# Optimization experiments

Hardware: AMD Instinct MI355X
Metric: run time of the kernel (lower is better)

## Reference

```python
import jax, jax.numpy as jnp
import numpy as np

B = 512       # batch
D = 256       # n_embd
NH = 4        # heads
NN = 8 * D // NH   # neurons per head = 512
NTOT = NH * NN     # 2048
DH = D // NH       # 64
K = 8              # thinking steps
EPS_LN = 1e-5


def _ln(x, g, b):
    mu = jnp.mean(x, axis=-1, keepdims=True)
    var = jnp.mean((x - mu) ** 2, axis=-1, keepdims=True)
    return (x - mu) * jax.lax.rsqrt(var + EPS_LN) * g + b


def setup_inputs() -> dict:
    key = jax.random.key(0)
    ks = jax.random.split(key, 12)
    s = 0.02
    w = lambda k, shape: (jax.random.normal(k, shape, jnp.float32) * s)
    return {
        "boards": jax.random.normal(ks[0], (B, 12, 8, 8), jnp.float32),
        # board_encoder: Linear(768,d) -> GELU -> LN(d) -> Linear(d,d); weights stored (in,out)
        "enc_w1": w(ks[1], (768, D)), "enc_b1": jnp.zeros((D,), jnp.float32),
        "enc_ln_g": jnp.ones((D,), jnp.float32), "enc_ln_b": jnp.zeros((D,), jnp.float32),
        "enc_w2": w(ks[2], (D, D)), "enc_b2": jnp.zeros((D,), jnp.float32),
        "xinit_w": w(ks[3], (D, NTOT)), "xinit_b": jnp.zeros((NTOT,), jnp.float32),
        "D_y": w(ks[4], (NH, D, NN)),
        "E": w(ks[5], (NTOT, D)),
        "D_x": w(ks[6], (NH, D, NN)),
        "By_w": w(ks[7], (D, D)),
        "Bx_w": w(ks[8], (D, D)),
        "lna_g": jnp.ones((D,), jnp.float32), "lna_b": jnp.zeros((D,), jnp.float32),
        "lnz_g": jnp.ones((D,), jnp.float32), "lnz_b": jnp.zeros((D,), jnp.float32),
        "log_damping": jnp.asarray(np.log(0.9 / 0.1), jnp.float32),
        "vh_w1": w(ks[9], (D, D // 2)), "vh_b1": jnp.zeros((D // 2,), jnp.float32),
        "vh_w2": w(ks[10], (D // 2, 1)), "vh_b2": jnp.zeros((1,), jnp.float32),
    }


def reference(boards, enc_w1, enc_b1, enc_ln_g, enc_ln_b, enc_w2, enc_b2,
              xinit_w, xinit_b, D_y, E, D_x, By_w, Bx_w,
              lna_g, lna_b, lnz_g, lnz_b, log_damping,
              vh_w1, vh_b1, vh_w2, vh_b2):
    Bn = boards.shape[0]
    flat = boards.reshape(Bn, 768)
    h = jax.nn.gelu(flat @ enc_w1 + enc_b1, approximate=False)
    h = _ln(h, enc_ln_g, enc_ln_b)
    b = h @ enc_w2 + enc_b2                      # (B, d)
    x0 = jax.nn.relu(b @ xinit_w + xinit_b)      # (B, n)
    rho0 = jnp.zeros((Bn, NH, NN, DH), boards.dtype)
    lam = jax.nn.sigmoid(log_damping)
    b_y = b @ By_w
    b_x = b @ Bx_w

    def step(carry, _):
        x, rho = carry
        x_h = x.reshape(Bn, NH, NN)
        a = jnp.einsum('bhnd,bhn->bhd', rho, x_h).reshape(Bn, D)   # read from scratchpad
        a_cond = _ln(a + b_y, lna_g, lna_b)
        g = jax.nn.relu(jnp.einsum('bd,hdn->bhn', a_cond, D_y))
        y = (g * x_h).reshape(Bn, NTOT)
        z = _ln(y @ E, lnz_g, lnz_b)
        dx = jax.nn.relu(jnp.einsum('bd,hdn->bhn', z + b_x, D_x))
        x_new = x + dx.reshape(Bn, NTOT)
        xh = x_new.reshape(Bn, NH, NN)
        x_write = xh / (jnp.linalg.norm(xh, axis=-1, keepdims=True) + 1e-8)
        z_h = z.reshape(Bn, NH, DH)
        rho_new = lam * rho + (1.0 - lam) * jnp.einsum('bhn,bhd->bhnd', x_write, z_h)
        return (x_new, rho_new), z

    (_, _), zs = jax.lax.scan(step, (x0, rho0), None, length=K)
    z_last = zs[-1]                              # (B, d) from final thinking step
    v = jnp.tanh(jax.nn.gelu(z_last @ vh_w1 + vh_b1, approximate=False) @ vh_w2 + vh_b2)
    return v                                     # (B, 1)
```

## Files before the change

kernel.cpp:

```cpp
#include <hip/hip_runtime.h>
#include <hip/hip_bf16.h>
#include <math.h>

#define B_ 512
#define D_ 256
#define NH_ 4
#define NN_ 512
#define NTOT_ 2048
#define DH_ 64
#define KSTEPS 8

typedef __attribute__((ext_vector_type(8))) short bf16x8;
typedef __attribute__((ext_vector_type(4))) float f32x4;

#if __has_builtin(__builtin_amdgcn_global_load_lds)
#define HAVE_GLL 1
#else
#define HAVE_GLL 0
#endif

__device__ __forceinline__ float gelu_exact(float x) {
  return 0.5f * x * (1.0f + erff(x * 0.70710678118654752f));
}

__device__ __forceinline__ unsigned short f2b(float f) {
  union { float f; unsigned int u; } x; x.f = f;
  unsigned int u = x.u;
  unsigned int r = (u + 0x7FFFu + ((u >> 16) & 1u)) >> 16;
  return (unsigned short)r;
}

__device__ __forceinline__ float blockReduceSum256(float v, float* red) {
  int t = threadIdx.x;
  red[t] = v; __syncthreads();
  #pragma unroll
  for (int st = 128; st > 0; st >>= 1) {
    if (t < st) red[t] += red[t + st];
    __syncthreads();
  }
  float r = red[0];
  __syncthreads();
  return r;
}

#if HAVE_GLL
__device__ __forceinline__ void load16_lds(const unsigned short* g, unsigned short* l) {
  __builtin_amdgcn_global_load_lds(
      (const __attribute__((address_space(1))) unsigned int*)g,
      (__attribute__((address_space(3))) unsigned int*)l, 16, 0, 0);
}
#endif

template<int EPI>
__global__ __launch_bounds__(256) void gemm_mfma(
    const unsigned short* __restrict__ A, const unsigned short* __restrict__ W,
    const float* __restrict__ bias, const float* __restrict__ mul,
    const float* __restrict__ addto, float* __restrict__ outf,
    unsigned short* __restrict__ outb, int K, int N, int kchunk)
{
  __shared__ __align__(16) unsigned short As[2][64 * 64];
  __shared__ __align__(16) unsigned short Ws[2][32 * 64];
  const int t = threadIdx.x;
  const int lane = t & 63;
  const int w = t >> 6;
  const int row0 = blockIdx.y * 64, col0 = blockIdx.x * 32;
  const int k0 = blockIdx.z * kchunk;
  const int nt = kchunk >> 6;
  const int lr = lane & 15, lk = lane >> 4;
  const int l3 = lane >> 3, cch = lane & 7;

  f32x4 acc[2];
  acc[0] = (f32x4){0.f, 0.f, 0.f, 0.f};
  acc[1] = (f32x4){0.f, 0.f, 0.f, 0.f};

#if HAVE_GLL
  #define STAGE(tt)                                                              \
    {                                                                            \
      int buf_ = (tt) & 1;                                                       \
      int kk_ = k0 + (tt) * 64;                                                  \
      _Pragma("unroll")                                                          \
      for (int p = 0; p < 2; p++) {                                              \
        int r_ = (w * 2 + p) * 8 + l3;                                           \
        load16_lds(&A[(size_t)(row0 + r_) * K + kk_ + ((cch ^ (r_ & 7)) << 3)],  \
                   &As[buf_][(w * 2 + p) * 512]);                                \
      }                                                                          \
      int rw_ = w * 8 + l3;                                                      \
      load16_lds(&W[(size_t)(col0 + rw_) * K + kk_ + ((cch ^ (rw_ & 7)) << 3)],  \
                 &Ws[buf_][w * 512]);                                            \
    }

  STAGE(0);
  for (int tt = 0; tt < nt; tt++) {
    asm volatile("s_waitcnt vmcnt(0)" ::: "memory");
    __builtin_amdgcn_s_barrier();
    asm volatile("" ::: "memory");
    if (tt + 1 < nt) STAGE(tt + 1);
    const unsigned short* Ab = As[tt & 1];
    const unsigned short* Wb = Ws[tt & 1];
    #pragma unroll
    for (int ks = 0; ks < 2; ks++) {
      int q = ks * 4 + lk;
      int r = w * 16 + lr;
      bf16x8 af = *(const bf16x8*)&Ab[r * 64 + ((q ^ (r & 7)) << 3)];
      #pragma unroll
      for (int j = 0; j < 2; j++) {
        int c = j * 16 + lr;
        bf16x8 bf = *(const bf16x8*)&Wb[c * 64 + ((q ^ (c & 7)) << 3)];
        acc[j] = __builtin_amdgcn_mfma_f32_16x16x32_bf16(af, bf, acc[j], 0, 0, 0);
      }
    }
  }
  #undef STAGE
#else
  for (int tt = 0; tt < nt; tt++) {
    int buf_ = tt & 1;
    int kk_ = k0 + tt * 64;
    #pragma unroll
    for (int p = 0; p < 2; p++) {
      int r_ = (w * 2 + p) * 8 + l3;
      bf16x8 v = *(const bf16x8*)&A[(size_t)(row0 + r_) * K + kk_ + ((cch ^ (r_ & 7)) << 3)];
      *(bf16x8*)&As[buf_][r_ * 64 + (cch << 3)] = v;
    }
    int rw_ = w * 8 + l3;
    bf16x8 vw = *(const bf16x8*)&W[(size_t)(col0 + rw_) * K + kk_ + ((cch ^ (rw_ & 7)) << 3)];
    *(bf16x8*)&Ws[buf_][rw_ * 64 + (cch << 3)] = vw;
    __syncthreads();
    const unsigned short* Ab = As[buf_];
    const unsigned short* Wb = Ws[buf_];
    #pragma unroll
    for (int ks = 0; ks < 2; ks++) {
      int q = ks * 4 + lk;
      int r = w * 16 + lr;
      bf16x8 af = *(const bf16x8*)&Ab[r * 64 + ((q ^ (r & 7)) << 3)];
      #pragma unroll
      for (int j = 0; j < 2; j++) {
        int c = j * 16 + lr;
        bf16x8 bf = *(const bf16x8*)&Wb[c * 64 + ((q ^ (c & 7)) << 3)];
        acc[j] = __builtin_amdgcn_mfma_f32_16x16x32_bf16(af, bf, acc[j], 0, 0, 0);
      }
    }
    __syncthreads();
  }
#endif

  const int cr = lk * 4;
  #pragma unroll
  for (int j = 0; j < 2; j++) {
    #pragma unroll
    for (int q = 0; q < 4; q++) {
      int r = row0 + w * 16 + cr + q;
      int c = col0 + j * 16 + lr;
      float v = acc[j][q];
      if (EPI == 0) {
        v += bias[c]; v = fmaxf(v, 0.f);
        outf[(size_t)r * N + c] = v;
      } else if (EPI == 1) {
        v = fmaxf(v, 0.f) * mul[(size_t)r * N + c];
        outb[(size_t)r * N + c] = f2b(v);
      } else if (EPI == 2) {
        outf[(size_t)blockIdx.z * ((size_t)512 * N) + (size_t)r * N + c] = v;
      } else {
        v = fmaxf(v, 0.f) + addto[(size_t)r * N + c];
        outf[(size_t)r * N + c] = v;
      }
    }
  }
}

template<int ACT>
__global__ __launch_bounds__(256) void gemm_tile(
    const float* __restrict__ A, const float* __restrict__ W,
    const float* __restrict__ bias, float* __restrict__ out,
    unsigned short* __restrict__ outb, int M, int N, int K, int kchunk)
{
  __shared__ float As[16][68];
  __shared__ float Bs[16][68];
  const int tid = threadIdx.x;
  const int row0 = blockIdx.y * 64;
  const int col0 = blockIdx.x * 64;
  const int k0 = blockIdx.z * kchunk;
  const int ty = tid >> 4, tx = tid & 15;
  const int ar = tid >> 4, ak = tid & 15;
  const int br = tid >> 6, bc = tid & 63;
  float acc[4][4] = {};
  for (int kk = k0; kk < k0 + kchunk; kk += 16) {
    #pragma unroll
    for (int i = 0; i < 4; i++) {
      int r = ar + i * 16;
      As[ak][r] = A[(size_t)(row0 + r) * K + kk + ak];
    }
    #pragma unroll
    for (int i = 0; i < 4; i++) {
      int kr = br + i * 4;
      Bs[kr][bc] = W[(size_t)(kk + kr) * N + col0 + bc];
    }
    __syncthreads();
    #pragma unroll
    for (int q = 0; q < 16; q++) {
      float4 av = *(const float4*)&As[q][ty * 4];
      float4 bv = *(const float4*)&Bs[q][tx * 4];
      float aa[4] = {av.x, av.y, av.z, av.w};
      float bb[4] = {bv.x, bv.y, bv.z, bv.w};
      #pragma unroll
      for (int i = 0; i < 4; i++)
        #pragma unroll
        for (int j = 0; j < 4; j++)
          acc[i][j] = fmaf(aa[i], bb[j], acc[i][j]);
    }
    __syncthreads();
  }
  const bool parts = (gridDim.z > 1);
  float* o = out + (parts ? (size_t)blockIdx.z * (size_t)M * N : (size_t)0);
  #pragma unroll
  for (int i = 0; i < 4; i++) {
    int r = row0 + ty * 4 + i;
    #pragma unroll
    for (int j = 0; j < 4; j++) {
      int c = col0 + tx * 4 + j;
      float v = acc[i][j];
      if (!parts) {
        if (bias) v += bias[c];
        if (ACT == 2) v = gelu_exact(v);
      }
      o[(size_t)r * N + c] = v;
      if (!parts && outb) outb[(size_t)r * N + c] = f2b(v);
    }
  }
}

__global__ __launch_bounds__(256) void k_prep(
    const float* __restrict__ D_y, const float* __restrict__ D_x,
    const float* __restrict__ xinit_w, const float* __restrict__ E,
    unsigned short* __restrict__ DyT, unsigned short* __restrict__ DxT,
    unsigned short* __restrict__ xinitT, unsigned short* __restrict__ ET)
{
  __shared__ float T[64][65];
  const float* in; unsigned short* out; int Kd, Nd, head, nx;
  switch (blockIdx.y) {
    case 0:  in = D_y;     out = DyT;    Kd = 256;  Nd = 2048; head = 1; nx = 32; break;
    case 1:  in = D_x;     out = DxT;    Kd = 256;  Nd = 2048; head = 1; nx = 32; break;
    case 2:  in = xinit_w; out = xinitT; Kd = 256;  Nd = 2048; head = 0; nx = 32; break;
    default: in = E;       out = ET;     Kd = 2048; Nd = 256;  head = 0; nx = 4;  break;
  }
  const int n0 = (blockIdx.x % nx) * 64, k0 = (blockIdx.x / nx) * 64;
  const int tx = threadIdx.x & 63, ty = threadIdx.x >> 6;
  #pragma unroll
  for (int i = 0; i < 16; i++) {
    int k = k0 + ty + i * 4;
    int n = n0 + tx;
    float v;
    if (head) v = in[((size_t)(n >> 9) * 256 + k) * 512 + (n & 511)];
    else      v = in[(size_t)k * Nd + n];
    T[ty + i * 4][tx] = v;
  }
  __syncthreads();
  #pragma unroll
  for (int i = 0; i < 16; i++) {
    int n = n0 + ty + i * 4;
    out[(size_t)n * Kd + k0 + tx] = f2b(T[tx][ty + i * 4]);
  }
}

__global__ __launch_bounds__(256) void k_ln_reduce(
    const float* __restrict__ in, int nparts, int stride,
    const float* __restrict__ pre_bias, int do_gelu,
    const float* __restrict__ g, const float* __restrict__ bta,
    const float* __restrict__ addvec, float* __restrict__ out,
    unsigned short* __restrict__ out2_bf)
{
  __shared__ float red[256];
  int b = blockIdx.x, d = threadIdx.x;
  float v = 0.f;
  for (int p = 0; p < nparts; p++) v += in[(size_t)p * stride + (size_t)b * 256 + d];
  if (pre_bias) v += pre_bias[d];
  if (do_gelu) v = gelu_exact(v);
  float mu = blockReduceSum256(v, red) * (1.f / 256.f);
  float c = v - mu;
  float var = blockReduceSum256(c * c, red) * (1.f / 256.f);
  float vn = c * rsqrtf(var + 1e-5f) * g[d] + bta[d];
  out[(size_t)b * 256 + d] = vn;
  if (out2_bf) out2_bf[(size_t)b * 256 + d] = f2b(vn + addvec[(size_t)b * 256 + d]);
}

__global__ __launch_bounds__(256) void step_a(
    const float* __restrict__ x, float* __restrict__ xw_hist,
    const float* __restrict__ z_hist, const float* __restrict__ b_y,
    const float* __restrict__ lna_g, const float* __restrict__ lna_b,
    const float* __restrict__ log_damp, int k, unsigned short* __restrict__ out)
{
  __shared__ float dots[KSTEPS][NH_];
  __shared__ float red[256];
  int b = blockIdx.x, t = threadIdx.x;
  int lane = t & 63, wv = t >> 6;
  float lam = 1.f / (1.f + expf(-log_damp[0]));
  const float* xb = x + (size_t)b * NTOT_;
  float xv[8];
  #pragma unroll
  for (int i = 0; i < 8; i++) xv[i] = xb[t * 8 + i];

  if (k >= 1) {
    float s = 0.f;
    #pragma unroll
    for (int i = 0; i < 8; i++) s += xv[i] * xv[i];
    #pragma unroll
    for (int m = 1; m < 64; m <<= 1) s += __shfl_xor(s, m, 64);
    float inv = 1.f / (sqrtf(s) + 1e-8f);
    float* xwout = xw_hist + ((size_t)(k - 1) * B_ + b) * NTOT_;
    #pragma unroll
    for (int i = 0; i < 8; i++) xwout[t * 8 + i] = xv[i] * inv;
    if (lane == 0) dots[k - 1][wv] = s * inv;
  }
  for (int j = 0; j < k - 1; j++) {
    const float* xwb = xw_hist + ((size_t)j * B_ + b) * NTOT_;
    float s = 0.f;
    #pragma unroll
    for (int i = 0; i < 8; i++) s += xv[i] * xwb[t * 8 + i];
    #pragma unroll
    for (int off = 32; off > 0; off >>= 1) s += __shfl_down(s, off, 64);
    if (lane == 0) dots[j][wv] = s;
  }
  __syncthreads();

  int d = t;
  float av = 0.f, lp = 1.f;
  for (int j = k - 1; j >= 0; j--) {
    av += (1.f - lam) * lp * dots[j][d >> 6] * z_hist[((size_t)j * B_ + b) * D_ + d];
    lp *= lam;
  }
  av += b_y[(size_t)b * D_ + d];
  float mu = blockReduceSum256(av, red) * (1.f / 256.f);
  float c = av - mu;
  float var = blockReduceSum256(c * c, red) * (1.f / 256.f);
  out[(size_t)b * D_ + d] = f2b(c * rsqrtf(var + 1e-5f) * lna_g[d] + lna_b[d]);
}

__global__ __launch_bounds__(128) void k_value(
    const float* __restrict__ z, const float* __restrict__ w1,
    const float* __restrict__ b1, const float* __restrict__ w2,
    const float* __restrict__ b2, float* __restrict__ out)
{
  __shared__ float red[128];
  int b = blockIdx.x, j = threadIdx.x;
  const float* zr = z + (size_t)b * 256;
  float s = 0.f;
  #pragma unroll 8
  for (int i = 0; i < 256; i++) s += zr[i] * w1[(size_t)i * 128 + j];
  float g = gelu_exact(s + b1[j]) * w2[j];
  red[j] = g; __syncthreads();
  #pragma unroll
  for (int st = 64; st > 0; st >>= 1) {
    if (j < st) red[j] += red[j + st];
    __syncthreads();
  }
  if (j == 0) out[b] = tanhf(red[0] + b2[0]);
}

extern "C" void kernel_launch(void* const* d_in, const int* in_sizes, int n_in,
                              void* d_out, int out_size, void* d_ws, size_t ws_size,
                              hipStream_t stream) {
  const float* boards   = (const float*)d_in[0];
  const float* enc_w1   = (const float*)d_in[1];
  const float* enc_b1   = (const float*)d_in[2];
  const float* enc_ln_g = (const float*)d_in[3];
  const float* enc_ln_b = (const float*)d_in[4];
  const float* enc_w2   = (const float*)d_in[5];
  const float* enc_b2   = (const float*)d_in[6];
  const float* xinit_w  = (const float*)d_in[7];
  const float* xinit_b  = (const float*)d_in[8];
  const float* D_y      = (const float*)d_in[9];
  const float* E        = (const float*)d_in[10];
  const float* D_x      = (const float*)d_in[11];
  const float* By_w     = (const float*)d_in[12];
  const float* Bx_w     = (const float*)d_in[13];
  const float* lna_g    = (const float*)d_in[14];
  const float* lna_b    = (const float*)d_in[15];
  const float* lnz_g    = (const float*)d_in[16];
  const float* lnz_b    = (const float*)d_in[17];
  const float* log_damp = (const float*)d_in[18];
  const float* vh_w1    = (const float*)d_in[19];
  const float* vh_b1    = (const float*)d_in[20];
  const float* vh_w2    = (const float*)d_in[21];
  const float* vh_b2    = (const float*)d_in[22];
  float* outp = (float*)d_out;

  float* ws = (float*)d_ws;
  size_t o = 0;
  float* x      = ws + o; o += (size_t)B_ * NTOT_;
  float* xw     = ws + o; o += (size_t)KSTEPS * B_ * NTOT_;
  float* zh     = ws + o; o += (size_t)KSTEPS * B_ * D_;
  float* hparts = ws + o; o += (size_t)8 * B_ * D_;
  float* h      = ws + o; o += (size_t)B_ * D_;
  float* bvec   = ws + o; o += (size_t)B_ * D_;
  float* b_y    = ws + o; o += (size_t)B_ * D_;
  float* b_x    = ws + o; o += (size_t)B_ * D_;
  float* zparts = ws + o; o += (size_t)8 * B_ * D_;
  unsigned short* DyT     = (unsigned short*)(ws + o); o += (size_t)NTOT_ * D_ / 2;
  unsigned short* DxT     = (unsigned short*)(ws + o); o += (size_t)NTOT_ * D_ / 2;
  unsigned short* ET      = (unsigned short*)(ws + o); o += (size_t)D_ * NTOT_ / 2;
  unsigned short* xinitT  = (unsigned short*)(ws + o); o += (size_t)NTOT_ * D_ / 2;
  unsigned short* bvec_bf = (unsigned short*)(ws + o); o += (size_t)B_ * D_ / 2;
  unsigned short* acond_bf= (unsigned short*)(ws + o); o += (size_t)B_ * D_ / 2;
  unsigned short* zbx_bf  = (unsigned short*)(ws + o); o += (size_t)B_ * D_ / 2;
  unsigned short* y_bf    = (unsigned short*)(ws + o); o += (size_t)B_ * NTOT_ / 2;

  k_prep<<<dim3(128, 4), 256, 0, stream>>>(D_y, D_x, xinit_w, E, DyT, DxT, xinitT, ET);

  gemm_tile<0><<<dim3(4, 8, 8), 256, 0, stream>>>(boards, enc_w1, nullptr, hparts,
                                                  nullptr, B_, D_, 768, 96);
  k_ln_reduce<<<B_, 256, 0, stream>>>(hparts, 8, B_ * D_, enc_b1, 1,
                                      enc_ln_g, enc_ln_b, nullptr, h, nullptr);
  gemm_tile<0><<<dim3(4, 8, 1), 256, 0, stream>>>(h, enc_w2, enc_b2, bvec, bvec_bf,
                                                  B_, D_, D_, D_);
  gemm_tile<0><<<dim3(4, 8, 1), 256, 0, stream>>>(bvec, By_w, nullptr, b_y, nullptr,
                                                  B_, D_, D_, D_);
  gemm_tile<0><<<dim3(4, 8, 1), 256, 0, stream>>>(bvec, Bx_w, nullptr, b_x, nullptr,
                                                  B_, D_, D_, D_);
  gemm_mfma<0><<<dim3(64, 8, 1), 256, 0, stream>>>(bvec_bf, xinitT, xinit_b, nullptr,
                                                   nullptr, x, nullptr, 256, 2048, 256);

  for (int k = 0; k < KSTEPS; k++) {
    step_a<<<B_, 256, 0, stream>>>(x, xw, zh, b_y, lna_g, lna_b, log_damp, k, acond_bf);
    gemm_mfma<1><<<dim3(64, 8, 1), 256, 0, stream>>>(acond_bf, DyT, nullptr, x,
                                                     nullptr, nullptr, y_bf, 256, 2048, 256);
    gemm_mfma<2><<<dim3(8, 8, 8), 256, 0, stream>>>(y_bf, ET, nullptr, nullptr,
                                                    nullptr, zparts, nullptr, 2048, 256, 256);
    k_ln_reduce<<<B_, 256, 0, stream>>>(zparts, 8, B_ * D_, nullptr, 0, lnz_g, lnz_b,
                                        b_x, zh + (size_t)k * B_ * D_, zbx_bf);
    gemm_mfma<3><<<dim3(64, 8, 1), 256, 0, stream>>>(zbx_bf, DxT, nullptr, nullptr,
                                                     x, x, nullptr, 256, 2048, 256);
  }

  k_value<<<B_, 128, 0, stream>>>(zh + (size_t)(KSTEPS - 1) * B_ * D_,
                                  vh_w1, vh_b1, vh_w2, vh_b2, outp);
}
```

Baseline: 413.7 us.

## Fuse thinking-loop kernels into one persistent kernel with grid barriers

Replaces the per-step launches (step_a, three MFMA GEMMs, LN reduce) and the final value head with a single persistent 256-block kernel. Phases are separated by atomic-counter grid barriers, which removes roughly forty kernel launches and their gaps. The By/Bx projections are merged into one GEMM over a concatenated weight, the E GEMM split-K drops from 8 to 4 partitions, and the last step skips the unused D_x update. The design relies on all 256 blocks being co-resident, or the spin barrier deadlocks, and each barrier adds spin and fence cost.

```diff
diff --git a/kernel.cpp b/kernel.cpp
--- a/kernel.cpp
+++ b/kernel.cpp
@@ -9,6 +9,7 @@
 #define NTOT_ 2048
 #define DH_ 64
 #define KSTEPS 8
+#define NBLK 256u
 
 typedef __attribute__((ext_vector_type(8))) short bf16x8;
 typedef __attribute__((ext_vector_type(4))) float f32x4;
@@ -30,19 +31,6 @@
   return (unsigned short)r;
 }
 
-__device__ __forceinline__ float blockReduceSum256(float v, float* red) {
-  int t = threadIdx.x;
-  red[t] = v; __syncthreads();
-  #pragma unroll
-  for (int st = 128; st > 0; st >>= 1) {
-    if (t < st) red[t] += red[t + st];
-    __syncthreads();
-  }
-  float r = red[0];
-  __syncthreads();
-  return r;
-}
-
 #if HAVE_GLL
 __device__ __forceinline__ void load16_lds(const unsigned short* g, unsigned short* l) {
   __builtin_amdgcn_global_load_lds(
@@ -51,90 +39,105 @@
 }
 #endif
 
-template<int EPI>
-__global__ __launch_bounds__(256) void gemm_mfma(
+__device__ __forceinline__ void gridbar(unsigned* bar, unsigned bi) {
+  __syncthreads();
+  if (threadIdx.x == 0) {
+    __threadfence();
+    atomicAdd(bar, 1u);
+    const unsigned target = (bi + 1u) * NBLK;
+    while (__hip_atomic_load(bar, __ATOMIC_RELAXED, __HIP_MEMORY_SCOPE_AGENT) < target)
+      __builtin_amdgcn_s_sleep(1);
+    __threadfence();
+  }
+  __syncthreads();
+}
+
+__device__ __forceinline__ float halfReduce(float v, float* red, int half, int tid) {
+  red[half * 256 + tid] = v; __syncthreads();
+  #pragma unroll
+  for (int st = 128; st > 0; st >>= 1) {
+    if (tid < st) red[half * 256 + tid] += red[half * 256 + tid + st];
+    __syncthreads();
+  }
+  float r = red[half * 256];
+  __syncthreads();
+  return r;
+}
+
+template<int JF, int EPI>
+__device__ __forceinline__ void gemm_phase(
     const unsigned short* __restrict__ A, const unsigned short* __restrict__ W,
-    const float* __restrict__ bias, const float* __restrict__ mul,
-    const float* __restrict__ addto, float* __restrict__ outf,
-    unsigned short* __restrict__ outb, int K, int N, int kchunk)
-{
-  __shared__ __align__(16) unsigned short As[2][64 * 64];
-  __shared__ __align__(16) unsigned short Ws[2][32 * 64];
+    const float* __restrict__ bias, const float* __restrict__ auxf,
+    float* __restrict__ outf, unsigned short* __restrict__ outb,
+    int K, int N, int m0, int n0, int k0, int nt, size_t partoff,
+    unsigned short* As, unsigned short* Ws)
+{
   const int t = threadIdx.x;
-  const int lane = t & 63;
-  const int w = t >> 6;
-  const int row0 = blockIdx.y * 64, col0 = blockIdx.x * 32;
-  const int k0 = blockIdx.z * kchunk;
-  const int nt = kchunk >> 6;
+  const int lane = t & 63, w = t >> 6;
   const int lr = lane & 15, lk = lane >> 4;
   const int l3 = lane >> 3, cch = lane & 7;
-
-  f32x4 acc[2];
-  acc[0] = (f32x4){0.f, 0.f, 0.f, 0.f};
-  acc[1] = (f32x4){0.f, 0.f, 0.f, 0.f};
+  const int wr = (w & 3) * 16;
+  const int wc = (w >> 2) * (JF * 16);
+  const int BN = JF * 32;
+
+  f32x4 acc[JF];
+  #pragma unroll
+  for (int j = 0; j < JF; j++) acc[j] = (f32x4){0.f, 0.f, 0.f, 0.f};
 
 #if HAVE_GLL
-  #define STAGE(tt)                                                              \
-    {                                                                            \
-      int buf_ = (tt) & 1;                                                       \
-      int kk_ = k0 + (tt) * 64;                                                  \
-      _Pragma("unroll")                                                          \
-      for (int p = 0; p < 2; p++) {                                              \
-        int r_ = (w * 2 + p) * 8 + l3;                                           \
-        load16_lds(&A[(size_t)(row0 + r_) * K + kk_ + ((cch ^ (r_ & 7)) << 3)],  \
-                   &As[buf_][(w * 2 + p) * 512]);                                \
-      }                                                                          \
-      int rw_ = w * 8 + l3;                                                      \
-      load16_lds(&W[(size_t)(col0 + rw_) * K + kk_ + ((cch ^ (rw_ & 7)) << 3)],  \
-                 &Ws[buf_][w * 512]);                                            \
-    }
-
-  STAGE(0);
+  #define STG(tt)                                                                   \
+    {                                                                               \
+      int buf_ = (tt) & 1; int kk_ = k0 + (tt) * 64;                                \
+      { int r_ = w * 8 + l3;                                                        \
+        load16_lds(&A[(size_t)(m0 + r_) * K + kk_ + ((cch ^ (r_ & 7)) << 3)],       \
+                   &As[buf_ * 4096 + w * 512]); }                                   \
+      if (w < BN / 8) { int r_ = w * 8 + l3;                                        \
+        load16_lds(&W[(size_t)(n0 + r_) * K + kk_ + ((cch ^ (r_ & 7)) << 3)],       \
+                   &Ws[buf_ * 4096 + w * 512]); }                                   \
+    }
+  STG(0);
   for (int tt = 0; tt < nt; tt++) {
     asm volatile("s_waitcnt vmcnt(0)" ::: "memory");
     __builtin_amdgcn_s_barrier();
     asm volatile("" ::: "memory");
-    if (tt + 1 < nt) STAGE(tt + 1);
-    const unsigned short* Ab = As[tt & 1];
-    const unsigned short* Wb = Ws[tt & 1];
+    if (tt + 1 < nt) STG(tt + 1);
+    const unsigned short* Ab = &As[(tt & 1) * 4096];
+    const unsigned short* Wb = &Ws[(tt & 1) * 4096];
     #pragma unroll
     for (int ks = 0; ks < 2; ks++) {
       int q = ks * 4 + lk;
-      int r = w * 16 + lr;
+      int r = wr + lr;
       bf16x8 af = *(const bf16x8*)&Ab[r * 64 + ((q ^ (r & 7)) << 3)];
       #pragma unroll
-      for (int j = 0; j < 2; j++) {
-        int c = j * 16 + lr;
+      for (int j = 0; j < JF; j++) {
+        int c = wc + j * 16 + lr;
         bf16x8 bf = *(const bf16x8*)&Wb[c * 64 + ((q ^ (c & 7)) << 3)];
         acc[j] = __builtin_amdgcn_mfma_f32_16x16x32_bf16(af, bf, acc[j], 0, 0, 0);
       }
     }
   }
-  #undef STAGE
+  #undef STG
 #else
   for (int tt = 0; tt < nt; tt++) {
-    int buf_ = tt & 1;
-    int kk_ = k0 + tt * 64;
-    #pragma unroll
-    for (int p = 0; p < 2; p++) {
-      int r_ = (w * 2 + p) * 8 + l3;
-      bf16x8 v = *(const bf16x8*)&A[(size_t)(row0 + r_) * K + kk_ + ((cch ^ (r_ & 7)) << 3)];
-      *(bf16x8*)&As[buf_][r_ * 64 + (cch << 3)] = v;
-    }
-    int rw_ = w * 8 + l3;
-    bf16x8 vw = *(const bf16x8*)&W[(size_t)(col0 + rw_) * K + kk_ + ((cch ^ (rw_ & 7)) << 3)];
-    *(bf16x8*)&Ws[buf_][rw_ * 64 + (cch << 3)] = vw;
+    int buf_ = tt & 1; int kk_ = k0 + tt * 64;
+    int r_ = w * 8 + l3;
+    bf16x8 va = *(const bf16x8*)&A[(size_t)(m0 + r_) * K + kk_ + ((cch ^ (r_ & 7)) << 3)];
+    *(bf16x8*)&As[buf_ * 4096 + r_ * 64 + (cch << 3)] = va;
+    if (w < BN / 8) {
+      bf16x8 vw = *(const bf16x8*)&W[(size_t)(n0 + r_) * K + kk_ + ((cch ^ (r_ & 7)) << 3)];
+      *(bf16x8*)&Ws[buf_ * 4096 + r_ * 64 + (cch << 3)] = vw;
+    }
     __syncthreads();
-    const unsigned short* Ab = As[buf_];
-    const unsigned short* Wb = Ws[buf_];
+    const unsigned short* Ab = &As[buf_ * 4096];
+    const unsigned short* Wb = &Ws[buf_ * 4096];
     #pragma unroll
     for (int ks = 0; ks < 2; ks++) {
       int q = ks * 4 + lk;
-      int r = w * 16 + lr;
+      int r = wr + lr;
       bf16x8 af = *(const bf16x8*)&Ab[r * 64 + ((q ^ (r & 7)) << 3)];
       #pragma unroll
-      for (int j = 0; j < 2; j++) {
-        int c = j * 16 + lr;
+      for (int j = 0; j < JF; j++) {
+        int c = wc + j * 16 + lr;
         bf16x8 bf = *(const bf16x8*)&Wb[c * 64 + ((q ^ (c & 7)) << 3)];
         acc[j] = __builtin_amdgcn_mfma_f32_16x16x32_bf16(af, bf, acc[j], 0, 0, 0);
       }
@@ -143,28 +146,174 @@
   }
 #endif
 
-  const int cr = lk * 4;
-  #pragma unroll
-  for (int j = 0; j < 2; j++) {
+  #pragma unroll
+  for (int j = 0; j < JF; j++) {
     #pragma unroll
     for (int q = 0; q < 4; q++) {
-      int r = row0 + w * 16 + cr + q;
-      int c = col0 + j * 16 + lr;
+      int r = m0 + wr + lk * 4 + q;
+      int c = n0 + wc + j * 16 + lr;
       float v = acc[j][q];
       if (EPI == 0) {
         v += bias[c]; v = fmaxf(v, 0.f);
         outf[(size_t)r * N + c] = v;
       } else if (EPI == 1) {
-        v = fmaxf(v, 0.f) * mul[(size_t)r * N + c];
+        v = fmaxf(v, 0.f) * auxf[(size_t)r * N + c];
         outb[(size_t)r * N + c] = f2b(v);
       } else if (EPI == 2) {
-        outf[(size_t)blockIdx.z * ((size_t)512 * N) + (size_t)r * N + c] = v;
+        outf[partoff + (size_t)r * N + c] = v;
       } else {
-        v = fmaxf(v, 0.f) + addto[(size_t)r * N + c];
+        v = fmaxf(v, 0.f) + auxf[(size_t)r * N + c];
         outf[(size_t)r * N + c] = v;
       }
     }
   }
+}
+
+__device__ __forceinline__ void phase_step_a(
+    int blk, const float* __restrict__ x, float* __restrict__ xw,
+    const float* __restrict__ zh, const float* __restrict__ bybx,
+    const float* lna_g, const float* lna_b, float lam, int k,
+    unsigned short* __restrict__ acond_bf, float* red, float* dots)
+{
+  const int t = threadIdx.x;
+  const int tid = t & 255, half = t >> 8;
+  const int b = blk * 2 + half;
+  const int lane = tid & 63, hd = tid >> 6;
+  const float* xb = x + (size_t)b * NTOT_;
+  float xv[8];
+  #pragma unroll
+  for (int i = 0; i < 8; i++) xv[i] = xb[tid * 8 + i];
+
+  if (k >= 1) {
+    float s = 0.f;
+    #pragma unroll
+    for (int i = 0; i < 8; i++) s += xv[i] * xv[i];
+    #pragma unroll
+    for (int m = 1; m < 64; m <<= 1) s += __shfl_xor(s, m, 64);
+    float inv = 1.f / (sqrtf(s) + 1e-8f);
+    float* xwo = xw + ((size_t)(k - 1) * B_ + b) * NTOT_;
+    #pragma unroll
+    for (int i = 0; i < 8; i++) xwo[tid * 8 + i] = xv[i] * inv;
+    if (lane == 0) dots[half * 32 + (k - 1) * 4 + hd] = s * inv;
+  }
+  for (int j = 0; j < k - 1; j++) {
+    const float* xwb = xw + ((size_t)j * B_ + b) * NTOT_;
+    float s = 0.f;
+    #pragma unroll
+    for (int i = 0; i < 8; i++) s += xv[i] * xwb[tid * 8 + i];
+    #pragma unroll
+    for (int off = 32; off > 0; off >>= 1) s += __shfl_down(s, off, 64);
+    if (lane == 0) dots[half * 32 + j * 4 + hd] = s;
+  }
+  __syncthreads();
+
+  int d = tid;
+  float av = 0.f, lp = 1.f;
+  for (int j = k - 1; j >= 0; j--) {
+    av += (1.f - lam) * lp * dots[half * 32 + j * 4 + (d >> 6)] *
+          zh[((size_t)j * B_ + b) * D_ + d];
+    lp *= lam;
+  }
+  av += bybx[(size_t)b * 512 + d];
+  float mu = halfReduce(av, red, half, tid) * (1.f / 256.f);
+  float c = av - mu;
+  float var = halfReduce(c * c, red, half, tid) * (1.f / 256.f);
+  acond_bf[(size_t)b * D_ + d] = f2b(c * rsqrtf(var + 1e-5f) * lna_g[d] + lna_b[d]);
+}
+
+__device__ __forceinline__ void phase_ln(
+    int blk, int k, const float* __restrict__ zparts, const float* __restrict__ bybx,
+    const float* lnz_g, const float* lnz_b, float* __restrict__ zh,
+    unsigned short* __restrict__ zbx_bf, float* red)
+{
+  const int t = threadIdx.x, tid = t & 255, half = t >> 8;
+  const int b = blk * 2 + half, d = tid;
+  float v = 0.f;
+  #pragma unroll
+  for (int p = 0; p < 4; p++) v += zparts[(size_t)p * (B_ * D_) + (size_t)b * D_ + d];
+  float mu = halfReduce(v, red, half, tid) * (1.f / 256.f);
+  float c = v - mu;
+  float var = halfReduce(c * c, red, half, tid) * (1.f / 256.f);
+  float vn = c * rsqrtf(var + 1e-5f) * lnz_g[d] + lnz_b[d];
+  zh[((size_t)k * B_ + b) * D_ + d] = vn;
+  zbx_bf[(size_t)b * D_ + d] = f2b(vn + bybx[(size_t)b * 512 + 256 + d]);
+}
+
+__device__ __forceinline__ void phase_value(
+    int blk, const float* __restrict__ z, const float* __restrict__ w1,
+    const float* __restrict__ b1, const float* __restrict__ w2,
+    const float* __restrict__ b2, float* __restrict__ out, float* red)
+{
+  const int t = threadIdx.x, tid = t & 255, half = t >> 8;
+  const int b = blk * 2 + half;
+  const int j = tid & 127, ih = tid >> 7;
+  const float* zr = z + (size_t)b * 256;
+  float s = 0.f;
+  #pragma unroll 4
+  for (int i = ih * 128; i < ih * 128 + 128; i++) s += zr[i] * w1[(size_t)i * 128 + j];
+  red[half * 256 + tid] = s; __syncthreads();
+  if (tid < 128) {
+    float sv = red[half * 256 + tid] + red[half * 256 + tid + 128] + b1[j];
+    red[half * 256 + tid] = gelu_exact(sv) * w2[tid];
+  }
+  __syncthreads();
+  #pragma unroll
+  for (int st = 64; st > 0; st >>= 1) {
+    if (tid < st) red[half * 256 + tid] += red[half * 256 + tid + st];
+    __syncthreads();
+  }
+  if (tid == 0) out[b] = tanhf(red[half * 256] + b2[0]);
+}
+
+__global__ __launch_bounds__(512, 2) void k_loop(
+    const unsigned short* __restrict__ bvec_bf, const unsigned short* __restrict__ xinitT,
+    const unsigned short* __restrict__ DyT, const unsigned short* __restrict__ DxT,
+    const unsigned short* __restrict__ ET,
+    const float* __restrict__ xinit_b, const float* __restrict__ bybx,
+    const float* __restrict__ lna_g, const float* __restrict__ lna_b,
+    const float* __restrict__ lnz_g, const float* __restrict__ lnz_b,
+    const float* __restrict__ log_damp,
+    const float* __restrict__ vh_w1, const float* __restrict__ vh_b1,
+    const float* __restrict__ vh_w2, const float* __restrict__ vh_b2,
+    float* __restrict__ x, float* __restrict__ xw, float* __restrict__ zh,
+    float* __restrict__ zparts, unsigned short* __restrict__ acond_bf,
+    unsigned short* __restrict__ y_bf, unsigned short* __restrict__ zbx_bf,
+    float* __restrict__ out, unsigned* __restrict__ bar)
+{
+  __shared__ __align__(16) unsigned short As[2 * 4096];
+  __shared__ __align__(16) unsigned short Ws[2 * 4096];
+  __shared__ float red[512];
+  __shared__ float dots[64];
+  const int blk = blockIdx.x;
+  const int mt = (blk >> 5) * 64;
+  const int n64 = (blk & 31) * 64;
+  const int rem = blk & 31;
+  const int nz = (rem >> 2) * 32, kz = rem & 3;
+  unsigned bi = 0;
+  const float lam = 1.f / (1.f + expf(-log_damp[0]));
+
+  gemm_phase<2, 0>(bvec_bf, xinitT, xinit_b, nullptr, x, nullptr,
+                   256, 2048, mt, n64, 0, 4, 0, As, Ws);
+  gridbar(bar, bi++);
+
+  for (int k = 0; k < KSTEPS; k++) {
+    phase_step_a(blk, x, xw, zh, bybx, lna_g, lna_b, lam, k, acond_bf, red, dots);
+    gridbar(bar, bi++);
+    gemm_phase<2, 1>(acond_bf, DyT, nullptr, x, nullptr, y_bf,
+                     256, 2048, mt, n64, 0, 4, 0, As, Ws);
+    gridbar(bar, bi++);
+    gemm_phase<1, 2>(y_bf, ET, nullptr, nullptr, zparts, nullptr,
+                     2048, 256, mt, nz, kz * 512, 8, (size_t)kz * (B_ * D_), As, Ws);
+    gridbar(bar, bi++);
+    phase_ln(blk, k, zparts, bybx, lnz_g, lnz_b, zh, zbx_bf, red);
+    gridbar(bar, bi++);
+    if (k < KSTEPS - 1) {
+      gemm_phase<2, 3>(zbx_bf, DxT, nullptr, x, x, nullptr,
+                       256, 2048, mt, n64, 0, 4, 0, As, Ws);
+      gridbar(bar, bi++);
+    }
+  }
+  phase_value(blk, zh + (size_t)(KSTEPS - 1) * B_ * D_, vh_w1, vh_b1, vh_w2, vh_b2, out, red);
 }
 
 template<int ACT>
@@ -231,9 +380,26 @@
 __global__ __launch_bounds__(256) void k_prep(
     const float* __restrict__ D_y, const float* __restrict__ D_x,
     const float* __restrict__ xinit_w, const float* __restrict__ E,
+    const float* __restrict__ By_w, const float* __restrict__ Bx_w,
     unsigned short* __restrict__ DyT, unsigned short* __restrict__ DxT,
-    unsigned short* __restrict__ xinitT, unsigned short* __restrict__ ET)
-{
+    unsigned short* __restrict__ xinitT, unsigned short* __restrict__ ET,
+    float* __restrict__ Wcat, unsigned* __restrict__ bar)
+{
+  const int t = threadIdx.x;
+  if (blockIdx.y == 4) {
+    if (blockIdx.x == 0 && t == 0) *bar = 0u;
+    if (blockIdx.x >= 32) return;
+    int k0 = ((int)blockIdx.x >> 3) * 64, n0 = ((int)blockIdx.x & 7) * 64;
+    for (int i = 0; i < 16; i++) {
+      int local = i * 256 + t;
+      int kk = local >> 6, nn = local & 63;
+      int n = n0 + nn;
+      float v = (n < 256) ? By_w[(size_t)(k0 + kk) * 256 + n]
+                          : Bx_w[(size_t)(k0 + kk) * 256 + (n - 256)];
+      Wcat[(size_t)(k0 + kk) * 512 + n] = v;
+    }
+    return;
+  }
   __shared__ float T[64][65];
   const float* in; unsigned short* out; int Kd, Nd, head, nx;
   switch (blockIdx.y) {
@@ -242,8 +408,8 @@
     case 2:  in = xinit_w; out = xinitT; Kd = 256;  Nd = 2048; head = 0; nx = 32; break;
     default: in = E;       out = ET;     Kd = 2048; Nd = 256;  head = 0; nx = 4;  break;
   }
-  const int n0 = (blockIdx.x % nx) * 64, k0 = (blockIdx.x / nx) * 64;
-  const int tx = threadIdx.x & 63, ty = threadIdx.x >> 6;
+  const int n0 = ((int)blockIdx.x % nx) * 64, k0 = ((int)blockIdx.x / nx) * 64;
+  const int tx = t & 63, ty = t >> 6;
   #pragma unroll
   for (int i = 0; i < 16; i++) {
     int k = k0 + ty + i * 4;
@@ -261,98 +427,27 @@
   }
 }
 
-__global__ __launch_bounds__(256) void k_ln_reduce(
+__global__ __launch_bounds__(256) void k_ln_enc(
     const float* __restrict__ in, int nparts, int stride,
-    const float* __restrict__ pre_bias, int do_gelu,
+    const float* __restrict__ pre_bias,
     const float* __restrict__ g, const float* __restrict__ bta,
-    const float* __restrict__ addvec, float* __restrict__ out,
-    unsigned short* __restrict__ out2_bf)
+    float* __restrict__ out)
 {
   __shared__ float red[256];
   int b = blockIdx.x, d = threadIdx.x;
   float v = 0.f;
   for (int p = 0; p < nparts; p++) v += in[(size_t)p * stride + (size_t)b * 256 + d];
-  if (pre_bias) v += pre_bias[d];
-  if (do_gelu) v = gelu_exact(v);
-  float mu = blockReduceSum256(v, red) * (1.f / 256.f);
+  v = gelu_exact(v + pre_bias[d]);
+  red[d] = v; __syncthreads();
+  #pragma unroll
+  for (int st = 128; st > 0; st >>= 1) { if (d < st) red[d] += red[d + st]; __syncthreads(); }
+  float mu = red[0] * (1.f / 256.f); __syncthreads();
   float c = v - mu;
-  float var = blockReduceSum256(c * c, red) * (1.f / 256.f);
-  float vn = c * rsqrtf(var + 1e-5f) * g[d] + bta[d];
-  out[(size_t)b * 256 + d] = vn;
-  if (out2_bf) out2_bf[(size_t)b * 256 + d] = f2b(vn + addvec[(size_t)b * 256 + d]);
-}
-
-__global__ __launch_bounds__(256) void step_a(
-    const float* __restrict__ x, float* __restrict__ xw_hist,
-    const float* __restrict__ z_hist, const float* __restrict__ b_y,
-    const float* __restrict__ lna_g, const float* __restrict__ lna_b,
-    const float* __restrict__ log_damp, int k, unsigned short* __restrict__ out)
-{
-  __shared__ float dots[KSTEPS][NH_];
-  __shared__ float red[256];
-  int b = blockIdx.x, t = threadIdx.x;
-  int lane = t & 63, wv = t >> 6;
-  float lam = 1.f / (1.f + expf(-log_damp[0]));
-  const float* xb = x + (size_t)b * NTOT_;
-  float xv[8];
-  #pragma unroll
-  for (int i = 0; i < 8; i++) xv[i] = xb[t * 8 + i];
-
-  if (k >= 1) {
-    float s = 0.f;
-    #pragma unroll
-    for (int i = 0; i < 8; i++) s += xv[i] * xv[i];
-    #pragma unroll
-    for (int m = 1; m < 64; m <<= 1) s += __shfl_xor(s, m, 64);
-    float inv = 1.f / (sqrtf(s) + 1e-8f);
-    float* xwout = xw_hist + ((size_t)(k - 1) * B_ + b) * NTOT_;
-    #pragma unroll
-    for (int i = 0; i < 8; i++) xwout[t * 8 + i] = xv[i] * inv;
-    if (lane == 0) dots[k - 1][wv] = s * inv;
-  }
-  for (int j = 0; j < k - 1; j++) {
-    const float* xwb = xw_hist + ((size_t)j * B_ + b) * NTOT_;
-    float s = 0.f;
-    #pragma unroll
-    for (int i = 0; i < 8; i++) s += xv[i] * xwb[t * 8 + i];
-    #pragma unroll
-    for (int off = 32; off > 0; off >>= 1) s += __shfl_down(s, off, 64);
-    if (lane == 0) dots[j][wv] = s;
-  }
-  __syncthreads();
-
-  int d = t;
-  float av = 0.f, lp = 1.f;
-  for (int j = k - 1; j >= 0; j--) {
-    av += (1.f - lam) * lp * dots[j][d >> 6] * z_hist[((size_t)j * B_ + b) * D_ + d];
-    lp *= lam;
-  }
-  av += b_y[(size_t)b * D_ + d];
-  float mu = blockReduceSum256(av, red) * (1.f / 256.f);
-  float c = av - mu;
-  float var = blockReduceSum256(c * c, red) * (1.f / 256.f);
-  out[(size_t)b * D_ + d] = f2b(c * rsqrtf(var + 1e-5f) * lna_g[d] + lna_b[d]);
-}
-
-__global__ __launch_bounds__(128) void k_value(
-    const float* __restrict__ z, const float* __restrict__ w1,
-    const float* __restrict__ b1, const float* __restrict__ w2,
-    const float* __restrict__ b2, float* __restrict__ out)
-{
-  __shared__ float red[128];
-  int b = blockIdx.x, j = threadIdx.x;
-  const float* zr = z + (size_t)b * 256;
-  float s = 0.f;
-  #pragma unroll 8
-  for (int i = 0; i < 256; i++) s += zr[i] * w1[(size_t)i * 128 + j];
-  float g = gelu_exact(s + b1[j]) * w2[j];
-  red[j] = g; __syncthreads();
-  #pragma unroll
-  for (int st = 64; st > 0; st >>= 1) {
-    if (j < st) red[j] += red[j + st];
-    __syncthreads();
-  }
-  if (j == 0) out[b] = tanhf(red[0] + b2[0]);
+  red[d] = c * c; __syncthreads();
+  #pragma unroll
+  for (int st = 128; st > 0; st >>= 1) { if (d < st) red[d] += red[d + st]; __syncthreads(); }
+  float var = red[0] * (1.f / 256.f);
+  out[(size_t)b * 256 + d] = c * rsqrtf(var + 1e-5f) * g[d] + bta[d];
 }
 
 extern "C" void kernel_launch(void* const* d_in, const int* in_sizes, int n_in,
@@ -391,9 +486,9 @@
   float* hparts = ws + o; o += (size_t)8 * B_ * D_;
   float* h      = ws + o; o += (size_t)B_ * D_;
   float* bvec   = ws + o; o += (size_t)B_ * D_;
-  float* b_y    = ws + o; o += (size_t)B_ * D_;
-  float* b_x    = ws + o; o += (size_t)B_ * D_;
-  float* zparts = ws + o; o += (size_t)8 * B_ * D_;
+  float* bybx   = ws + o; o += (size_t)B_ * 512;
+  float* Wcat   = ws + o; o += (size_t)256 * 512;
+  float* zparts = ws + o; o += (size_t)4 * B_ * D_;
   unsigned short* DyT     = (unsigned short*)(ws + o); o += (size_t)NTOT_ * D_ / 2;
   unsigned short* DxT     = (unsigned short*)(ws + o); o += (size_t)NTOT_ * D_ / 2;
   unsigned short* ET      = (unsigned short*)(ws + o); o += (size_t)D_ * NTOT_ / 2;
@@ -402,34 +497,20 @@
   unsigned short* acond_bf= (unsigned short*)(ws + o); o += (size_t)B_ * D_ / 2;
   unsigned short* zbx_bf  = (unsigned short*)(ws + o); o += (size_t)B_ * D_ / 2;
   unsigned short* y_bf    = (unsigned short*)(ws + o); o += (size_t)B_ * NTOT_ / 2;
-
-  k_prep<<<dim3(128, 4), 256, 0, stream>>>(D_y, D_x, xinit_w, E, DyT, DxT, xinitT, ET);
-
+  unsigned* bar           = (unsigned*)(ws + o); o += 64;
+
+  k_prep<<<dim3(128, 5), 256, 0, stream>>>(D_y, D_x, xinit_w, E, By_w, Bx_w,
+                                           DyT, DxT, xinitT, ET, Wcat, bar);
   gemm_tile<0><<<dim3(4, 8, 8), 256, 0, stream>>>(boards, enc_w1, nullptr, hparts,
                                                   nullptr, B_, D_, 768, 96);
-  k_ln_reduce<<<B_, 256, 0, stream>>>(hparts, 8, B_ * D_, enc_b1, 1,
-                                      enc_ln_g, enc_ln_b, nullptr, h, nullptr);
+  k_ln_enc<<<B_, 256, 0, stream>>>(hparts, 8, B_ * D_, enc_b1, enc_ln_g, enc_ln_b, h);
   gemm_tile<0><<<dim3(4, 8, 1), 256, 0, stream>>>(h, enc_w2, enc_b2, bvec, bvec_bf,
                                                   B_, D_, D_, D_);
-  gemm_tile<0><<<dim3(4, 8, 1), 256, 0, stream>>>(bvec, By_w, nullptr, b_y, nullptr,
-                                                  B_, D_, D_, D_);
-  gemm_tile<0><<<dim3(4, 8, 1), 256, 0, stream>>>(bvec, Bx_w, nullptr, b_x, nullptr,
-                                                  B_, D_, D_, D_);
-  gemm_mfma<0><<<dim3(64, 8, 1), 256, 0, stream>>>(bvec_bf, xinitT, xinit_b, nullptr,
-                                                   nullptr, x, nullptr, 256, 2048, 256);
-
-  for (int k = 0; k < KSTEPS; k++) {
-    step_a<<<B_, 256, 0, stream>>>(x, xw, zh, b_y, lna_g, lna_b, log_damp, k, acond_bf);
-    gemm_mfma<1><<<dim3(64, 8, 1), 256, 0, stream>>>(acond_bf, DyT, nullptr, x,
-                                                     nullptr, nullptr, y_bf, 256, 2048, 256);
-    gemm_mfma<2><<<dim3(8, 8, 8), 256, 0, stream>>>(y_bf, ET, nullptr, nullptr,
-                                                    nullptr, zparts, nullptr, 2048, 256, 256);
-    k_ln_reduce<<<B_, 256, 0, stream>>>(zparts, 8, B_ * D_, nullptr, 0, lnz_g, lnz_b,
-                                        b_x, zh + (size_t)k * B_ * D_, zbx_bf);
-    gemm_mfma<3><<<dim3(64, 8, 1), 256, 0, stream>>>(zbx_bf, DxT, nullptr, nullptr,
-                                                     x, x, nullptr, 256, 2048, 256);
-  }
-
-  k_value<<<B_, 128, 0, stream>>>(zh + (size_t)(KSTEPS - 1) * B_ * D_,
-                                  vh_w1, vh_b1, vh_w2, vh_b2, outp);
-}
+  gemm_tile<0><<<dim3(8, 8, 1), 256, 0, stream>>>(bvec, Wcat, nullptr, bybx, nullptr,
+                                                  B_, 512, D_, D_);
+  k_loop<<<NBLK, 512, 0, stream>>>(bvec_bf, xinitT, DyT, DxT, ET, xinit_b, bybx,
+                                   lna_g, lna_b, lnz_g, lnz_b, log_damp,
+                                   vh_w1, vh_b1, vh_w2, vh_b2,
+                                   x, xw, zh, zparts, acond_bf, y_bf, zbx_bf,
+                                   outp, bar);
+}
```

Result: slower. 1.148 ms (+177.4%).
